# Kernel tuning notes

Hardware: AMD Instinct MI355X
Metric: run time of the kernel (lower is better)

## Reference

```python
import jax, jax.numpy as jnp
import numpy as np

IN_BW = 4
W_BW = 4
EPS = 1e-5


def quantize(x, bw):
    # k-bit uniform quantizer on [-1, 1 - 2^(1-bw)] with straight-through rounding
    scale = 2.0 ** (bw - 1)
    xc = jnp.clip(x, -1.0, 1.0 - 1.0 / scale)
    q = jnp.round(xc * scale) / scale
    return xc + jax.lax.stop_gradient(q - xc)


def bconv(x, w, stride):
    # BinarizeConv2d: quantize activations (in_bw) and weights (weight_bw), then conv
    return jax.lax.conv_general_dilated(
        quantize(x, IN_BW), quantize(w, W_BW),
        window_strides=stride, padding='VALID',
        dimension_numbers=('NCHW', 'OIHW', 'NCHW'))


def bn2d(x, g, b):
    mean = x.mean(axis=(0, 2, 3), keepdims=True)
    var = x.var(axis=(0, 2, 3), keepdims=True)
    return (x - mean) * jax.lax.rsqrt(var + EPS) * g.reshape(1, -1, 1, 1) + b.reshape(1, -1, 1, 1)


def bn1d(x, g, b):
    mean = x.mean(axis=0, keepdims=True)
    var = x.var(axis=0, keepdims=True)
    return (x - mean) * jax.lax.rsqrt(var + EPS) * g + b


def htanh(x):
    return jnp.clip(x, -1.0, 1.0)


def setup_inputs() -> dict:
    key = jax.random.key(0)
    ks = jax.random.split(key, 24)
    B = 8192
    d = {'x': jax.random.normal(ks[0], (B, 1, 1250, 1), dtype=jnp.float32)}
    # conv weights OIHW
    shapes = [(3, 1, 6, 1), (5, 3, 5, 1), (10, 5, 4, 1), (20, 10, 4, 1), (20, 20, 4, 1)]
    for i, s in enumerate(shapes):
        d[f'w{i+1}'] = 0.3 * jax.random.normal(ks[1 + i], s, dtype=jnp.float32)
    d['fw1'] = 0.3 * jax.random.normal(ks[6], (10, 740), dtype=jnp.float32)
    d['fw2'] = 0.3 * jax.random.normal(ks[7], (2, 10), dtype=jnp.float32)
    chans = [3, 5, 10, 20, 20, 10, 2]
    for i, c in enumerate(chans):
        d[f'g{i+1}'] = 1.0 + 0.1 * jax.random.normal(ks[8 + i], (c,), dtype=jnp.float32)
        d[f'b{i+1}'] = 0.1 * jax.random.normal(ks[15 + i], (c,), dtype=jnp.float32)
    return d


def reference(x, w1, w2, w3, w4, w5, fw1, fw2,
              g1, g2, g3, g4, g5, g6, g7,
              b1, b2, b3, b4, b5, b6, b7):
    h = htanh(bn2d(bconv(x, w1, (2, 1)), g1, b1))
    h = htanh(bn2d(bconv(h, w2, (2, 1)), g2, b2))
    h = htanh(bn2d(bconv(h, w3, (2, 1)), g3, b3))
    h = htanh(bn2d(bconv(h, w4, (2, 1)), g4, b4))
    h = htanh(bn2d(bconv(h, w5, (2, 1)), g5, b5))
    h = h.reshape(h.shape[0], -1)  # (B, 20*37*1) = (B, 740)
    # dropout is identity in eval mode
    h = htanh(bn1d(quantize(h, IN_BW) @ quantize(fw1, W_BW).T, g6, b6))
    h = bn1d(quantize(h, IN_BW) @ quantize(fw2, W_BW).T, g7, b7)
    return h
```

## Files before the change

kernel.cpp:

```cpp
#include <hip/hip_runtime.h>

#define DEV __device__ __forceinline__

DEV float qwt(float w) {
    float y = fminf(fmaxf(w, -1.0f), 0.875f);
    return rintf(y * 8.0f) * 0.125f;
}
DEV int qw8i(float w) {
    float y = fminf(fmaxf(w, -1.0f), 0.875f);
    return (int)rintf(y * 8.0f);
}
DEV int q8i(float x, float a, float b) {
    float y = fmaf(x, a, b);
    y = fminf(fmaxf(y, -1.0f), 0.875f);
    return (int)rintf(y * 8.0f);
}
DEV float qact(float x, float a, float b) {
    float y = fmaf(x, a, b);
    y = fminf(fmaxf(y, -1.0f), 0.875f);
    return rintf(y * 8.0f) * 0.125f;
}

DEV int dot4(int a, int b, int c) {
#if __has_builtin(__builtin_amdgcn_sdot4)
    return __builtin_amdgcn_sdot4(a, b, c, false);
#else
    c += (int)(signed char)(a)       * (int)(signed char)(b);
    c += (int)(signed char)(a >> 8)  * (int)(signed char)(b >> 8);
    c += (int)(signed char)(a >> 16) * (int)(signed char)(b >> 16);
    c += (int)(signed char)(a >> 24) * (int)(signed char)(b >> 24);
    return c;
#endif
}
DEV unsigned alignpair(unsigned hi, unsigned lo, int bits) {
#if __has_builtin(__builtin_amdgcn_alignbit)
    return __builtin_amdgcn_alignbit(hi, lo, bits);
#else
    return bits ? ((lo >> bits) | (hi << (32 - bits))) : lo;
#endif
}

DEV void atomAddF64(double* p, double v) { atomicAdd(p, v); }

DEV void pack_layer(const float* w, int* o, int CIN, int COUT, int K, int t) {
    int KW = (K + 3) / 4;
    for (int i = t; i < COUT * CIN * KW; i += 256) {
        int j = i % KW, cc = i / KW;
        unsigned r = 0;
        for (int u = 0; u < 4; u++) {
            int k = 4 * j + u;
            int b = (k < K) ? (qw8i(w[cc * K + k]) & 0xff) : 0;
            r |= (unsigned)b << (8 * u);
        }
        o[i] = (int)r;
    }
}

template<int CIN,int COUT,int K,int LINP,int LOUT,int LOUTP,int P,int R,bool IN_FLOAT,int LIN=0>
DEV void conv_phase(
    const void* __restrict__ in_, const int* __restrict__ wqi,
    const double* __restrict__ statsIn,
    const float* __restrict__ gprev, const float* __restrict__ bprev, double Nprev,
    short* __restrict__ out, double* __restrict__ statsOut, int B, int VB,
    const float* __restrict__ wown,
    const float* __restrict__ pw2, const float* __restrict__ pw3,
    const float* __restrict__ pw4, const float* __restrict__ pw5,
    int* __restrict__ owp2, int* __restrict__ owp3,
    int* __restrict__ owp4, int* __restrict__ owp5)
{
    constexpr int KW   = (K + 3) / 4;
    constexpr int NE   = P + 2 * KW - 1;
    constexpr int ND   = (2 * (NE - 1) + 3) / 4 + 2;
    constexpr int LO_P = (LOUT + P - 1) / P;
    constexpr int GROUPS = R * LO_P;

    __shared__ __align__(16) signed char smem[R * CIN * LINP + 32];
    __shared__ float ts[CIN], tb[CIN];
    __shared__ float red[4][2 * COUT];
    __shared__ int lwq[IN_FLOAT ? (COUT * CIN * KW) : 1];

    const int tid = threadIdx.x;
    const int bid = blockIdx.x;
    const int lane = tid & 63, wid = tid >> 6;

    if constexpr (IN_FLOAT) {
        for (int i = tid; i < COUT * CIN * KW; i += 256) {
            int j = i % KW, cc = i / KW;
            unsigned rr = 0;
            for (int u = 0; u < 4; u++) {
                int k = 4 * j + u;
                int bv = (k < K) ? (qw8i(wown[cc * K + k]) & 0xff) : 0;
                rr |= (unsigned)bv << (8 * u);
            }
            lwq[i] = (int)rr;
        }
        if (bid == 0) {
            pack_layer(pw2, owp2, 3, 5, 5, tid);
            pack_layer(pw3, owp3, 5, 10, 4, tid);
            pack_layer(pw4, owp4, 10, 20, 4, tid);
            pack_layer(pw5, owp5, 20, 20, 4, tid);
        }
    } else {
        if (tid < CIN) {
            double S = 0.0, Q = 0.0;
#pragma unroll
            for (int s = 0; s < 8; s++) {
                S += statsIn[s * (2 * CIN) + 2 * tid];
                Q += statsIn[s * (2 * CIN) + 2 * tid + 1];
            }
            double mean = S / Nprev;
            double var  = Q / Nprev - mean * mean;
            double inv  = 1.0 / sqrt(var + 1e-5);
            double sc   = (double)gprev[tid] * inv;
            ts[tid] = (float)sc * 0.015625f;
            tb[tid] = (float)((double)bprev[tid] - mean * sc);
        }
    }
    __syncthreads();

#pragma unroll 1
    for (int vb = bid; vb < VB; vb += gridDim.x) {
        const int r0   = vb * R;
        const int rcnt = min(R, B - r0);

        if constexpr (IN_FLOAT) {
            constexpr int CH = LIN / 2;
            const float2* gp = (const float2*)in_;
            for (int c = tid; c < rcnt * CH; c += 256) {
                int r = c / CH, rem = c - r * CH;
                float2 v = gp[(size_t)(r0 + r) * CH + rem];
                int b0 = q8i(v.x, 1.f, 0.f) & 0xff;
                int b1 = q8i(v.y, 1.f, 0.f) & 0xff;
                *(unsigned short*)(smem + r * LINP + rem * 2) =
                    (unsigned short)(b0 | (b1 << 8));
            }
        } else {
            constexpr int CH  = CIN * LINP / 8;
            constexpr int CHC = LINP / 8;
            const int4* gp = (const int4*)((const short*)in_ + (size_t)r0 * CIN * LINP);
            for (int c = tid; c < rcnt * CH; c += 256) {
                int rem = c % CH;
                int ci = rem / CHC;
                float a = ts[ci], bo = tb[ci];
                int4 v = gp[c];
                int vs[4] = { v.x, v.y, v.z, v.w };
                unsigned pk[2];
#pragma unroll
                for (int u = 0; u < 2; u++) {
                    unsigned pp = 0;
#pragma unroll
                    for (int j = 0; j < 2; j++) {
                        int word = vs[u * 2 + j];
                        int b0 = q8i((float)(short)(word & 0xffff), a, bo) & 0xff;
                        int b1 = q8i((float)(short)(word >> 16),    a, bo) & 0xff;
                        pp |= (unsigned)(b0 | (b1 << 8)) << (16 * j);
                    }
                    pk[u] = pp;
                }
                ((uint2*)smem)[c] = make_uint2(pk[0], pk[1]);
            }
        }
        __syncthreads();

        float tsum[COUT], tsq[COUT];
#pragma unroll
        for (int c = 0; c < COUT; c++) { tsum[c] = 0.f; tsq[c] = 0.f; }

#pragma unroll 1
        for (int g = tid; g < GROUPS; g += 256) {
            int r = g / LO_P;
            if (r >= rcnt) continue;
            int l0   = (g - r * LO_P) * P;
            int pact = min(P, LOUT - l0);

            int acc[COUT][P];
#pragma unroll
            for (int co = 0; co < COUT; co++)
#pragma unroll
                for (int p = 0; p < P; p++) acc[co][p] = 0;

            const int ibase = r * CIN * LINP + 2 * l0;
            const int sh    = (P % 2 == 0) ? 0 : (ibase & 3);

            for (int ci = 0; ci < CIN; ci++) {
                const int* sp = (const int*)smem + ((ci * LINP + (ibase & ~3)) >> 2);
                int d[ND];
#pragma unroll
                for (int j = 0; j < ND; j++) d[j] = sp[j];
                int e[NE];
#pragma unroll
                for (int i = 0; i < NE; i++) {
                    int off = sh + 2 * i;
                    e[i] = (int)alignpair((unsigned)d[off / 4 + 1], (unsigned)d[off / 4], (off & 3) * 8);
                }
#pragma unroll
                for (int co = 0; co < COUT; co++) {
#pragma unroll
                    for (int j = 0; j < KW; j++) {
                        int wv;
                        if constexpr (IN_FLOAT) wv = lwq[(co * CIN + ci) * KW + j];
                        else                    wv = wqi[(co * CIN + ci) * KW + j];
#pragma unroll
                        for (int p = 0; p < P; p++)
                            acc[co][p] = dot4(e[p + 2 * j], wv, acc[co][p]);
                    }
                }
            }

            const size_t ob = (size_t)(r0 + r) * COUT * LOUTP + l0;
#pragma unroll
            for (int co = 0; co < COUT; co++) {
                if (pact == P) {
                    short tmp[P];
#pragma unroll
                    for (int p = 0; p < P; p++) {
                        tmp[p] = (short)acc[co][p];
                        float v = (float)acc[co][p] * 0.015625f;
                        tsum[co] += v;
                        tsq[co]   = fmaf(v, v, tsq[co]);
                    }
                    short* op = &out[ob + (size_t)co * LOUTP];
                    if constexpr (P == 1) {
                        op[0] = tmp[0];
                    } else if constexpr (P == 2) {
                        *(short2*)op = make_short2(tmp[0], tmp[1]);
                    } else if constexpr (P == 4) {
                        *(short4*)op = make_short4(tmp[0], tmp[1], tmp[2], tmp[3]);
                    } else if constexpr (P == 8) {
                        *(short4*)op       = make_short4(tmp[0], tmp[1], tmp[2], tmp[3]);
                        *(short4*)(op + 4) = make_short4(tmp[4], tmp[5], tmp[6], tmp[7]);
                    }
                } else {
#pragma unroll
                    for (int p = 0; p < P; p++) {
                        if (p < pact) {
                            int k = acc[co][p];
                            out[ob + (size_t)co * LOUTP + p] = (short)k;
                            float v = (float)k * 0.015625f;
                            tsum[co] += v;
                            tsq[co]   = fmaf(v, v, tsq[co]);
                        }
                    }
                }
            }
        }

#pragma unroll
        for (int co = 0; co < COUT; co++) {
            float s = tsum[co], q = tsq[co];
            for (int off = 32; off > 0; off >>= 1) {
                s += __shfl_down(s, off, 64);
                q += __shfl_down(q, off, 64);
            }
            if (lane == 0) { red[wid][2 * co] = s; red[wid][2 * co + 1] = q; }
        }
        __syncthreads();
        if (tid < 2 * COUT) {
            float v = red[0][tid] + red[1][tid] + red[2][tid] + red[3][tid];
            atomAddF64(&statsOut[(size_t)(vb & 7) * (2 * COUT) + tid], (double)v);
        }
        __syncthreads();
    }
}

__global__ __launch_bounds__(256) void k_conv1(
    const float* x, short* y1, double* sl1, int B, int VB,
    const float* w1, const float* w2, const float* w3, const float* w4,
    const float* w5, int* wp2, int* wp3, int* wp4, int* wp5)
{
    conv_phase<1, 3, 6, 1252, 623, 624, 8, 3, true, 1250>(
        x, nullptr, nullptr, nullptr, nullptr, 0.0, y1, sl1, B, VB,
        w1, w2, w3, w4, w5, wp2, wp3, wp4, wp5);
}
__global__ __launch_bounds__(256) void k_conv2(
    const short* in_, const int* wq, const double* sIn,
    const float* g, const float* b, short* out, double* sOut, int B, int VB)
{
    conv_phase<3, 5, 5, 624, 310, 312, 4, 4, false>(
        in_, wq, sIn, g, b, 8192.0 * 623.0, out, sOut, B, VB,
        nullptr, nullptr, nullptr, nullptr, nullptr, nullptr, nullptr, nullptr, nullptr);
}
__global__ __launch_bounds__(256) void k_conv3(
    const short* in_, const int* wq, const double* sIn,
    const float* g, const float* b, short* out, double* sOut, int B, int VB)
{
    conv_phase<5, 10, 4, 312, 154, 160, 2, 4, false>(
        in_, wq, sIn, g, b, 8192.0 * 310.0, out, sOut, B, VB,
        nullptr, nullptr, nullptr, nullptr, nullptr, nullptr, nullptr, nullptr, nullptr);
}
__global__ __launch_bounds__(256) void k_conv4(
    const short* in_, const int* wq, const double* sIn,
    const float* g, const float* b, short* out, double* sOut, int B, int VB)
{
    conv_phase<10, 20, 4, 160, 76, 80, 1, 4, false>(
        in_, wq, sIn, g, b, 8192.0 * 154.0, out, sOut, B, VB,
        nullptr, nullptr, nullptr, nullptr, nullptr, nullptr, nullptr, nullptr, nullptr);
}
__global__ __launch_bounds__(256) void k_conv5(
    const short* in_, const int* wq, const double* sIn,
    const float* g, const float* b, short* out, double* sOut, int B, int VB)
{
    conv_phase<20, 20, 4, 80, 37, 40, 1, 8, false>(
        in_, wq, sIn, g, b, 8192.0 * 76.0, out, sOut, B, VB,
        nullptr, nullptr, nullptr, nullptr, nullptr, nullptr, nullptr, nullptr, nullptr);
}

__global__ __launch_bounds__(256) void k_fc1(
    const short* __restrict__ y5, const float* __restrict__ fw1,
    const double* __restrict__ statsIn,
    const float* __restrict__ g5, const float* __restrict__ b5,
    float* __restrict__ z1, double* __restrict__ statsOut, int B)
{
    __shared__ float wq[7400];
    __shared__ float ts[20], tb[20];
    __shared__ float red[4][20];

    const int tid = threadIdx.x;
    const int bid = blockIdx.x;
    const int lane = tid & 63, wid = tid >> 6;

    for (int i = tid; i < 7400; i += 256) wq[i] = qwt(fw1[i]);
    if (tid < 20) {
        double S = 0.0, Q = 0.0;
#pragma unroll
        for (int s = 0; s < 8; s++) {
            S += statsIn[s * 40 + 2 * tid];
            Q += statsIn[s * 40 + 2 * tid + 1];
        }
        double N = 8192.0 * 37.0;
        double mean = S / N;
        double var  = Q / N - mean * mean;
        double inv  = 1.0 / sqrt(var + 1e-5);
        double sc   = (double)g5[tid] * inv;
        ts[tid] = (float)sc;
        tb[tid] = (float)((double)b5[tid] - mean * sc);
    }
    __syncthreads();

#pragma unroll 1
    for (int r = bid * 4 + wid; r < B; r += gridDim.x * 4) {
        const short* xr = y5 + (size_t)r * 800;
        float acc[10];
#pragma unroll
        for (int j = 0; j < 10; j++) acc[j] = 0.f;
#pragma unroll 1
        for (int f = lane; f < 740; f += 64) {
            int c = f / 37, pos = f - c * 37;
            float x = qact((float)xr[c * 40 + pos] * 0.015625f, ts[c], tb[c]);
#pragma unroll
            for (int j = 0; j < 10; j++) acc[j] = fmaf(x, wq[j * 740 + f], acc[j]);
        }
#pragma unroll
        for (int j = 0; j < 10; j++) {
            float v = acc[j];
            for (int off = 1; off < 64; off <<= 1) v += __shfl_xor(v, off, 64);
            if (lane == j) z1[(size_t)r * 10 + j] = v;
            if (lane == 0) { red[wid][2 * j] = v; red[wid][2 * j + 1] = v * v; }
        }
        __syncthreads();
        if (tid < 20) {
            float v = red[0][tid] + red[1][tid] + red[2][tid] + red[3][tid];
            atomAddF64(&statsOut[(size_t)(bid & 7) * 20 + tid], (double)v);
        }
        __syncthreads();
    }
}

__global__ __launch_bounds__(256) void k_fc2(
    const float* __restrict__ z1, const float* __restrict__ fw2,
    const double* __restrict__ statsIn,
    const float* __restrict__ g6, const float* __restrict__ b6,
    const float* __restrict__ g7, const float* __restrict__ b7,
    float* __restrict__ outp, int B)
{
    __shared__ float zbuf[16384];
    __shared__ float ts7[10], tb7[10], wq2[20];
    __shared__ float fr[4][4];
    __shared__ float tr8[4];

    const int tid = threadIdx.x;
    const int lane = tid & 63, wid = tid >> 6;

    if (tid < 20) wq2[tid] = qwt(fw2[tid]);
    if (tid < 10) {
        double S = 0.0, Q = 0.0;
#pragma unroll
        for (int s = 0; s < 8; s++) {
            S += statsIn[s * 20 + 2 * tid];
            Q += statsIn[s * 20 + 2 * tid + 1];
        }
        double N = 8192.0;
        double mean = S / N;
        double var  = Q / N - mean * mean;
        double inv  = 1.0 / sqrt(var + 1e-5);
        double sc   = (double)g6[tid] * inv;
        ts7[tid] = (float)sc;
        tb7[tid] = (float)((double)b6[tid] - mean * sc);
    }
    __syncthreads();

    float s0 = 0.f, q0 = 0.f, s1 = 0.f, q1 = 0.f;
#pragma unroll 1
    for (int r = tid; r < B; r += 256) {
        float a0 = 0.f, a1 = 0.f;
#pragma unroll
        for (int i = 0; i < 10; i++) {
            float x = qact(z1[(size_t)r * 10 + i], ts7[i], tb7[i]);
            a0 = fmaf(x, wq2[i], a0);
            a1 = fmaf(x, wq2[10 + i], a1);
        }
        zbuf[r * 2]     = a0;
        zbuf[r * 2 + 1] = a1;
        s0 += a0; q0 = fmaf(a0, a0, q0);
        s1 += a1; q1 = fmaf(a1, a1, q1);
    }
    for (int off = 32; off > 0; off >>= 1) {
        s0 += __shfl_down(s0, off, 64); q0 += __shfl_down(q0, off, 64);
        s1 += __shfl_down(s1, off, 64); q1 += __shfl_down(q1, off, 64);
    }
    if (lane == 0) { fr[wid][0] = s0; fr[wid][1] = q0; fr[wid][2] = s1; fr[wid][3] = q1; }
    __syncthreads();
    if (tid < 2) {
        double S = 0.0, Q = 0.0;
        for (int w = 0; w < 4; w++) { S += (double)fr[w][2 * tid]; Q += (double)fr[w][2 * tid + 1]; }
        double N = (double)B;
        double mean = S / N;
        double var  = Q / N - mean * mean;
        double inv  = 1.0 / sqrt(var + 1e-5);
        double sc   = (double)g7[tid] * inv;
        tr8[tid]     = (float)sc;
        tr8[2 + tid] = (float)((double)b7[tid] - mean * sc);
    }
    __syncthreads();
    for (int i = tid; i < 2 * B; i += 256) {
        int c = i & 1;
        outp[i] = fmaf(zbuf[i], tr8[c], tr8[2 + c]);
    }
}

extern "C" void kernel_launch(void* const* d_in, const int* in_sizes, int n_in,
                              void* d_out, int out_size, void* d_ws, size_t ws_size,
                              hipStream_t stream)
{
    const float* x   = (const float*)d_in[0];
    const float* w1  = (const float*)d_in[1];
    const float* w2  = (const float*)d_in[2];
    const float* w3  = (const float*)d_in[3];
    const float* w4  = (const float*)d_in[4];
    const float* w5  = (const float*)d_in[5];
    const float* fw1 = (const float*)d_in[6];
    const float* fw2 = (const float*)d_in[7];
    const float *g[7], *bb[7];
    for (int i = 0; i < 7; i++) { g[i] = (const float*)d_in[8 + 2 * i]; bb[i] = (const float*)d_in[9 + 2 * i]; }

    char* ws = (char*)d_ws;
    size_t off = 0;
    auto alloc = [&](size_t bytes) -> void* {
        void* q = ws + off;
        off += (bytes + 255) & ~(size_t)255;
        return q;
    };
    short* y1 = (short*)alloc((size_t)8192 * 3 * 624 * 2);
    short* y2 = (short*)alloc((size_t)8192 * 5 * 312 * 2);
    short* y3 = (short*)alloc((size_t)8192 * 10 * 160 * 2);
    short* y4 = (short*)alloc((size_t)8192 * 20 * 80 * 2);
    short* y5 = (short*)alloc((size_t)8192 * 20 * 40 * 2);
    float* z1 = (float*)alloc((size_t)81920 * 4);
    int*   wp2 = (int*)alloc(256);  int* wp3 = (int*)alloc(256);
    int*   wp4 = (int*)alloc(1024); int* wp5 = (int*)alloc(2048);
    double* slots = (double*)alloc((size_t)1088 * 8);
    double* sl1 = slots;
    double* sl2 = sl1 + 8 * 6;
    double* sl3 = sl2 + 8 * 10;
    double* sl4 = sl3 + 8 * 20;
    double* sl5 = sl4 + 8 * 40;
    double* sl6 = sl5 + 8 * 40;

    const int B = 8192;

    hipMemsetAsync(slots, 0, (size_t)1088 * 8, stream);

    k_conv1<<<512, 256, 0, stream>>>(x, y1, sl1, B, 2731,
                                     w1, w2, w3, w4, w5, wp2, wp3, wp4, wp5);
    k_conv2<<<512, 256, 0, stream>>>(y1, wp2, sl1, g[0], bb[0], y2, sl2, B, 2048);
    k_conv3<<<512, 256, 0, stream>>>(y2, wp3, sl2, g[1], bb[1], y3, sl3, B, 2048);
    k_conv4<<<512, 256, 0, stream>>>(y3, wp4, sl3, g[2], bb[2], y4, sl4, B, 2048);
    k_conv5<<<512, 256, 0, stream>>>(y4, wp5, sl4, g[3], bb[3], y5, sl5, B, 1024);
    k_fc1<<<1024, 256, 0, stream>>>(y5, fw1, sl5, g[4], bb[4], z1, sl6, B);
    k_fc2<<<1, 256, 0, stream>>>(z1, fw2, sl6, g[5], bb[5], g[6], bb[6],
                                 (float*)d_out, B);
}
```

Baseline: 338.2 us.

## Batch conv input loads, hoist fc1 stats reduction, unroll fc2, double grid sizes

The conv input staging loop now issues four global loads per thread before quantizing, to raise memory-level parallelism. fc1 keeps per-row BN statistics in registers and does a single shared reduction and atomic per block instead of two barriers and atomics per row. fc2 processes two rows per iteration, and launch grids for the conv and fc1 kernels are doubled. This costs more registers per thread and adds prologue work in the extra blocks, since each block re-quantizes its weights and recomputes stats at start.

```diff
diff --git a/kernel.cpp b/kernel.cpp
--- a/kernel.cpp
+++ b/kernel.cpp
@@ -126,38 +126,64 @@
         if constexpr (IN_FLOAT) {
             constexpr int CH = LIN / 2;
             const float2* gp = (const float2*)in_;
-            for (int c = tid; c < rcnt * CH; c += 256) {
-                int r = c / CH, rem = c - r * CH;
-                float2 v = gp[(size_t)(r0 + r) * CH + rem];
-                int b0 = q8i(v.x, 1.f, 0.f) & 0xff;
-                int b1 = q8i(v.y, 1.f, 0.f) & 0xff;
-                *(unsigned short*)(smem + r * LINP + rem * 2) =
-                    (unsigned short)(b0 | (b1 << 8));
+            const int total = rcnt * CH;
+#pragma unroll 1
+            for (int base = 0; base < total; base += 1024) {
+                float2 v[4];
+#pragma unroll
+                for (int u = 0; u < 4; u++) {
+                    int c = base + u * 256 + tid;
+                    if (c < total) v[u] = gp[(size_t)r0 * CH + c];
+                }
+#pragma unroll
+                for (int u = 0; u < 4; u++) {
+                    int c = base + u * 256 + tid;
+                    if (c < total) {
+                        int r = c / CH, rem = c - r * CH;
+                        int b0 = q8i(v[u].x, 1.f, 0.f) & 0xff;
+                        int b1 = q8i(v[u].y, 1.f, 0.f) & 0xff;
+                        *(unsigned short*)(smem + r * LINP + rem * 2) =
+                            (unsigned short)(b0 | (b1 << 8));
+                    }
+                }
             }
         } else {
             constexpr int CH  = CIN * LINP / 8;
             constexpr int CHC = LINP / 8;
             const int4* gp = (const int4*)((const short*)in_ + (size_t)r0 * CIN * LINP);
-            for (int c = tid; c < rcnt * CH; c += 256) {
-                int rem = c % CH;
-                int ci = rem / CHC;
-                float a = ts[ci], bo = tb[ci];
-                int4 v = gp[c];
-                int vs[4] = { v.x, v.y, v.z, v.w };
-                unsigned pk[2];
-#pragma unroll
-                for (int u = 0; u < 2; u++) {
-                    unsigned pp = 0;
-#pragma unroll
-                    for (int j = 0; j < 2; j++) {
-                        int word = vs[u * 2 + j];
-                        int b0 = q8i((float)(short)(word & 0xffff), a, bo) & 0xff;
-                        int b1 = q8i((float)(short)(word >> 16),    a, bo) & 0xff;
-                        pp |= (unsigned)(b0 | (b1 << 8)) << (16 * j);
+            const int total = rcnt * CH;
+#pragma unroll 1
+            for (int base = 0; base < total; base += 1024) {
+                int4 v[4];
+#pragma unroll
+                for (int u = 0; u < 4; u++) {
+                    int c = base + u * 256 + tid;
+                    if (c < total) v[u] = gp[c];
+                }
+#pragma unroll
+                for (int u = 0; u < 4; u++) {
+                    int c = base + u * 256 + tid;
+                    if (c < total) {
+                        int rem = c % CH;
+                        int ci = rem / CHC;
+                        float a = ts[ci], bo = tb[ci];
+                        int vs[4] = { v[u].x, v[u].y, v[u].z, v[u].w };
+                        unsigned pk[2];
+#pragma unroll
+                        for (int w8 = 0; w8 < 2; w8++) {
+                            unsigned pp = 0;
+#pragma unroll
+                            for (int j = 0; j < 2; j++) {
+                                int word = vs[w8 * 2 + j];
+                                int b0 = q8i((float)(short)(word & 0xffff), a, bo) & 0xff;
+                                int b1 = q8i((float)(short)(word >> 16),    a, bo) & 0xff;
+                                pp |= (unsigned)(b0 | (b1 << 8)) << (16 * j);
+                            }
+                            pk[w8] = pp;
+                        }
+                        ((uint2*)smem)[c] = make_uint2(pk[0], pk[1]);
                     }
-                    pk[u] = pp;
-                }
-                ((uint2*)smem)[c] = make_uint2(pk[0], pk[1]);
+                }
             }
         }
         __syncthreads();
@@ -317,7 +343,6 @@
 
     const int tid = threadIdx.x;
     const int bid = blockIdx.x;
-    const int lane = tid & 63, wid = tid >> 6;
 
     for (int i = tid; i < 7400; i += 256) wq[i] = qwt(fw1[i]);
     if (tid < 20) {
@@ -337,6 +362,11 @@
     }
     __syncthreads();
 
+    const int lane = tid & 63, wid = tid >> 6;
+    float tsum[10], tsq[10];
+#pragma unroll
+    for (int j = 0; j < 10; j++) { tsum[j] = 0.f; tsq[j] = 0.f; }
+
 #pragma unroll 1
     for (int r = bid * 4 + wid; r < B; r += gridDim.x * 4) {
         const short* xr = y5 + (size_t)r * 800;
@@ -354,15 +384,18 @@
         for (int j = 0; j < 10; j++) {
             float v = acc[j];
             for (int off = 1; off < 64; off <<= 1) v += __shfl_xor(v, off, 64);
+            tsum[j] += v; tsq[j] = fmaf(v, v, tsq[j]);
             if (lane == j) z1[(size_t)r * 10 + j] = v;
-            if (lane == 0) { red[wid][2 * j] = v; red[wid][2 * j + 1] = v * v; }
-        }
-        __syncthreads();
-        if (tid < 20) {
-            float v = red[0][tid] + red[1][tid] + red[2][tid] + red[3][tid];
-            atomAddF64(&statsOut[(size_t)(bid & 7) * 20 + tid], (double)v);
-        }
-        __syncthreads();
+        }
+    }
+    if (lane == 0) {
+#pragma unroll
+        for (int j = 0; j < 10; j++) { red[wid][2 * j] = tsum[j]; red[wid][2 * j + 1] = tsq[j]; }
+    }
+    __syncthreads();
+    if (tid < 20) {
+        float v = red[0][tid] + red[1][tid] + red[2][tid] + red[3][tid];
+        atomAddF64(&statsOut[(size_t)(bid & 7) * 20 + tid], (double)v);
     }
 }
 
@@ -401,18 +434,29 @@
 
     float s0 = 0.f, q0 = 0.f, s1 = 0.f, q1 = 0.f;
 #pragma unroll 1
-    for (int r = tid; r < B; r += 256) {
-        float a0 = 0.f, a1 = 0.f;
+    for (int r = tid; r < B; r += 512) {
+        const int r2 = r + 256;
+        float a0 = 0.f, a1 = 0.f, c0 = 0.f, c1 = 0.f;
 #pragma unroll
         for (int i = 0; i < 10; i++) {
-            float x = qact(z1[(size_t)r * 10 + i], ts7[i], tb7[i]);
-            a0 = fmaf(x, wq2[i], a0);
-            a1 = fmaf(x, wq2[10 + i], a1);
-        }
-        zbuf[r * 2]     = a0;
-        zbuf[r * 2 + 1] = a1;
+            float xA = qact(z1[(size_t)r * 10 + i], ts7[i], tb7[i]);
+            a0 = fmaf(xA, wq2[i], a0);
+            a1 = fmaf(xA, wq2[10 + i], a1);
+        }
+#pragma unroll
+        for (int i = 0; i < 10; i++) {
+            float xB = qact(z1[(size_t)r2 * 10 + i], ts7[i], tb7[i]);
+            c0 = fmaf(xB, wq2[i], c0);
+            c1 = fmaf(xB, wq2[10 + i], c1);
+        }
+        zbuf[r * 2]      = a0;
+        zbuf[r * 2 + 1]  = a1;
+        zbuf[r2 * 2]     = c0;
+        zbuf[r2 * 2 + 1] = c1;
         s0 += a0; q0 = fmaf(a0, a0, q0);
         s1 += a1; q1 = fmaf(a1, a1, q1);
+        s0 += c0; q0 = fmaf(c0, c0, q0);
+        s1 += c1; q1 = fmaf(c1, c1, q1);
     }
     for (int off = 32; off > 0; off >>= 1) {
         s0 += __shfl_down(s0, off, 64); q0 += __shfl_down(q0, off, 64);
@@ -480,13 +524,13 @@
 
     hipMemsetAsync(slots, 0, (size_t)1088 * 8, stream);
 
-    k_conv1<<<512, 256, 0, stream>>>(x, y1, sl1, B, 2731,
-                                     w1, w2, w3, w4, w5, wp2, wp3, wp4, wp5);
-    k_conv2<<<512, 256, 0, stream>>>(y1, wp2, sl1, g[0], bb[0], y2, sl2, B, 2048);
-    k_conv3<<<512, 256, 0, stream>>>(y2, wp3, sl2, g[1], bb[1], y3, sl3, B, 2048);
-    k_conv4<<<512, 256, 0, stream>>>(y3, wp4, sl3, g[2], bb[2], y4, sl4, B, 2048);
-    k_conv5<<<512, 256, 0, stream>>>(y4, wp5, sl4, g[3], bb[3], y5, sl5, B, 1024);
-    k_fc1<<<1024, 256, 0, stream>>>(y5, fw1, sl5, g[4], bb[4], z1, sl6, B);
+    k_conv1<<<1024, 256, 0, stream>>>(x, y1, sl1, B, 2731,
+                                      w1, w2, w3, w4, w5, wp2, wp3, wp4, wp5);
+    k_conv2<<<1024, 256, 0, stream>>>(y1, wp2, sl1, g[0], bb[0], y2, sl2, B, 2048);
+    k_conv3<<<1024, 256, 0, stream>>>(y2, wp3, sl2, g[1], bb[1], y3, sl3, B, 2048);
+    k_conv4<<<1024, 256, 0, stream>>>(y3, wp4, sl3, g[2], bb[2], y4, sl4, B, 2048);
+    k_conv5<<<1024, 256, 0, stream>>>(y4, wp5, sl4, g[3], bb[3], y5, sl5, B, 1024);
+    k_fc1<<<2048, 256, 0, stream>>>(y5, fw1, sl5, g[4], bb[4], z1, sl6, B);
     k_fc2<<<1, 256, 0, stream>>>(z1, fw2, sl6, g[5], bb[5], g[6], bb[6],
                                  (float*)d_out, B);
 }
```

New measurement: 286.9 us. -15.2%, faster.
